# Kernel tuning notes

Hardware: AMD Instinct MI355X
Metric: run time of the kernel (lower is better)

Reference implementation:

```python
import jax, jax.numpy as jnp
import numpy as np

E = 768
H = 12
D = E // H  # head_dim = 64
EPS = 1e-6
SCALE = D ** -0.5


def _l2norm(x, eps=EPS):
    # torch F.normalize: x / clamp_min(||x||_2, eps)
    n = jnp.sqrt(jnp.sum(x * x, axis=-1, keepdims=True))
    return x / jnp.maximum(n, eps)


def setup_inputs() -> dict:
    key = jax.random.key(0)
    ks = jax.random.split(key, 12)
    B, S = 2, 2048
    w = lambda k: jax.random.normal(k, (E, E), dtype=jnp.float32) * 0.02
    b = lambda k: jax.random.normal(k, (E,), dtype=jnp.float32) * 0.02
    return {
        "query": jax.random.normal(ks[0], (B, S, E), dtype=jnp.float32),
        "key": jax.random.normal(ks[1], (B, S, E), dtype=jnp.float32),
        "value": jax.random.normal(ks[2], (B, S, E), dtype=jnp.float32),
        "Wq": w(ks[3]), "bq": b(ks[4]),
        "Wk": w(ks[5]), "bk": b(ks[6]),
        "Wv": w(ks[7]), "bv": b(ks[8]),
        "Wo": w(ks[9]), "bo": b(ks[10]),
    }


def reference(query, key, value, Wq, bq, Wk, bk, Wv, bv, Wo, bo):
    B, T, _ = query.shape
    S = key.shape[1]
    # nn.Linear: x @ W.T + b; then split heads -> [B, H, S, D]
    split = lambda x, L: x.reshape(B, L, H, D).transpose(0, 2, 1, 3)
    q = split(query @ Wq.T + bq, T)
    k = split(key @ Wk.T + bk, S)
    v = split(value @ Wv.T + bv, S)
    q = _l2norm(q)
    k = _l2norm(k)
    scores = jnp.einsum("bhtd,bhsd->bhts", q, k) * SCALE
    attn = jax.nn.softmax(scores, axis=-1)
    ctx = jnp.einsum("bhts,bhsd->bhtd", attn, v)
    ctx = ctx.transpose(0, 2, 1, 3).reshape(B, T, E)
    return ctx @ Wo.T + bo
```

## Files before the change

kernel.cpp:

```cpp
#include <hip/hip_runtime.h>
#include <hip/hip_bf16.h>

#define EE 768
#define HH 12
#define DD 64
#define BB 2
#define SS 2048
#define MM (BB*SS)
#define NT (MM*EE)
#define NW (EE*EE)

typedef short short8 __attribute__((ext_vector_type(8)));
typedef float f32x4 __attribute__((ext_vector_type(4)));

static __device__ __forceinline__ unsigned short f2bf(float f) {
    unsigned int u = __float_as_uint(f);
    u += 0x7fffu + ((u >> 16) & 1u);
    return (unsigned short)(u >> 16);
}

static __device__ __forceinline__ void gl16(const void* g, void* l) {
    __builtin_amdgcn_global_load_lds(
        (const __attribute__((address_space(1))) unsigned int*)g,
        (__attribute__((address_space(3))) unsigned int*)l, 16, 0, 0);
}

static __device__ __forceinline__ int swz(int row, int chunk) {
    return row * 128 + ((chunk ^ (row & 7)) << 4);
}

__global__ __launch_bounds__(256) void cvt_all_kernel(
    const float* __restrict__ xq, const float* __restrict__ xk, const float* __restrict__ xv,
    const float* __restrict__ wq, const float* __restrict__ wk,
    const float* __restrict__ wv, const float* __restrict__ wo,
    unsigned short* __restrict__ oq, unsigned short* __restrict__ ok, unsigned short* __restrict__ ov,
    unsigned short* __restrict__ owq, unsigned short* __restrict__ owk,
    unsigned short* __restrict__ owv, unsigned short* __restrict__ owo)
{
    const int XQ = NT / 4;
    const int WQ = NW / 4;
    const int idx = blockIdx.x * 256 + threadIdx.x;
    const float* s;
    unsigned short* d;
    int off;
    if (idx < 3 * XQ) {
        const int r = idx / XQ;
        off = idx - r * XQ;
        s = (r == 0) ? xq : (r == 1) ? xk : xv;
        d = (r == 0) ? oq : (r == 1) ? ok : ov;
    } else {
        const int j = idx - 3 * XQ;
        const int r = j / WQ;
        off = j - r * WQ;
        s = (r == 0) ? wq : (r == 1) ? wk : (r == 2) ? wv : wo;
        d = (r == 0) ? owq : (r == 1) ? owk : (r == 2) ? owv : owo;
    }
    float4 f = ((const float4*)s)[off];
    ushort4 u;
    u.x = f2bf(f.x); u.y = f2bf(f.y); u.z = f2bf(f.z); u.w = f2bf(f.w);
    ((ushort4*)d)[off] = u;
}

static __device__ __forceinline__ void stage_ab(
    const unsigned short* __restrict__ x, const unsigned short* __restrict__ W,
    int bm, int n0, int kt, short* Abuf, short* Bbuf, int w, int lr8, int lc8)
{
    #pragma unroll
    for (int i = 0; i < 4; ++i) {
        const int t = w * 4 + i;
        gl16(x + (size_t)(bm + t * 8 + lr8) * EE + kt + lc8 * 8,
             (unsigned short*)Abuf + t * 512);
    }
    #pragma unroll
    for (int i = 0; i < 2; ++i) {
        const int t = w * 2 + i;
        gl16(W + (size_t)(n0 + t * 8 + lr8) * EE + kt + lc8 * 8,
             (unsigned short*)Bbuf + t * 512);
    }
}

__global__ __launch_bounds__(256) void qkv_mfma_kernel(
    const unsigned short* __restrict__ xq, const unsigned short* __restrict__ xk,
    const unsigned short* __restrict__ xv,
    const unsigned short* __restrict__ Wq, const float* __restrict__ bq,
    const unsigned short* __restrict__ Wk, const float* __restrict__ bk,
    const unsigned short* __restrict__ Wv, const float* __restrict__ bv,
    unsigned short* __restrict__ qo, unsigned short* __restrict__ ko,
    unsigned short* __restrict__ vo)
{
    __shared__ short As[2][128 * 64];
    __shared__ short Bs[2][64 * 64];
    __shared__ float ssq[2][128];

    const int tid = threadIdx.x;
    const int bm  = blockIdx.x * 128;
    const int by  = blockIdx.y;
    const int proj = by / 12;
    const int h    = by % 12;
    const int n0r  = h * 64;

    const unsigned short* x = (proj == 0) ? xq : (proj == 1) ? xk : xv;
    const unsigned short* W = (proj == 0) ? Wq : (proj == 1) ? Wk : Wv;
    const float* bias       = (proj == 0) ? bq : (proj == 1) ? bk : bv;

    const int w  = tid >> 6;
    const int l  = tid & 63;
    const int c  = l & 15;
    const int g  = l >> 4;
    const int wm = w >> 1;
    const int wn = w & 1;
    const int lr8 = l >> 3;
    const int lc8 = (l & 7) ^ lr8;

    f32x4 acc[4][2] = {};

    stage_ab(x, W, bm, n0r, 0, As[0], Bs[0], w, lr8, lc8);
    __syncthreads();

    for (int it = 0; it < EE / 64; ++it) {
        const int cur = it & 1;
        if (it + 1 < EE / 64)
            stage_ab(x, W, bm, n0r, (it + 1) * 64, As[cur ^ 1], Bs[cur ^ 1], w, lr8, lc8);

        #pragma unroll
        for (int ks = 0; ks < 2; ++ks) {
            short8 bfr[2], afr[4];
            #pragma unroll
            for (int nt = 0; nt < 2; ++nt)
                bfr[nt] = *(const short8*)((const char*)Bs[cur] + swz(wn * 32 + nt * 16 + c, ks * 4 + g));
            #pragma unroll
            for (int mt = 0; mt < 4; ++mt)
                afr[mt] = *(const short8*)((const char*)As[cur] + swz(wm * 64 + mt * 16 + c, ks * 4 + g));
            #pragma unroll
            for (int mt = 0; mt < 4; ++mt)
                #pragma unroll
                for (int nt = 0; nt < 2; ++nt)
                    acc[mt][nt] = __builtin_amdgcn_mfma_f32_16x16x32_bf16(
                        afr[mt], bfr[nt], acc[mt][nt], 0, 0, 0);
        }
        __syncthreads();
    }

    float bb[2];
    #pragma unroll
    for (int nt = 0; nt < 2; ++nt) bb[nt] = bias[n0r + wn * 32 + nt * 16 + c];

    const int bidx  = bm >> 11;
    const int sbase = bm & (SS - 1);

    if (proj < 2) {
        f32x4 vr[4][2];
        f32x4 ssp[4];
        #pragma unroll
        for (int mt = 0; mt < 4; ++mt) {
            #pragma unroll
            for (int nt = 0; nt < 2; ++nt)
                #pragma unroll
                for (int j = 0; j < 4; ++j)
                    vr[mt][nt][j] = acc[mt][nt][j] + bb[nt];
            #pragma unroll
            for (int j = 0; j < 4; ++j)
                ssp[mt][j] = vr[mt][0][j]*vr[mt][0][j] + vr[mt][1][j]*vr[mt][1][j];
            #pragma unroll
            for (int j = 0; j < 4; ++j) {
                float s = ssp[mt][j];
                #pragma unroll
                for (int msk = 1; msk < 16; msk <<= 1) s += __shfl_xor(s, msk);
                ssp[mt][j] = s;
            }
        }
        if (c == 0) {
            #pragma unroll
            for (int mt = 0; mt < 4; ++mt)
                #pragma unroll
                for (int j = 0; j < 4; ++j)
                    ssq[wn][wm * 64 + mt * 16 + g * 4 + j] = ssp[mt][j];
        }
        __syncthreads();
        unsigned short* dst = (proj == 0) ? qo : ko;
        const float fold = (proj == 0) ? 0.125f : 1.0f;
        #pragma unroll
        for (int mt = 0; mt < 4; ++mt) {
            #pragma unroll
            for (int j = 0; j < 4; ++j) {
                const int rloc = wm * 64 + mt * 16 + g * 4 + j;
                const float ss = ssq[0][rloc] + ssq[1][rloc];
                const float inv = fold / fmaxf(sqrtf(ss), 1e-6f);
                const size_t base =
                    ((size_t)(bidx * HH + h) * SS + sbase + rloc) * DD;
                #pragma unroll
                for (int nt = 0; nt < 2; ++nt)
                    dst[base + wn * 32 + nt * 16 + c] = f2bf(vr[mt][nt][j] * inv);
            }
        }
    } else {
        short* T = As[0];
        #pragma unroll
        for (int mt = 0; mt < 4; ++mt)
            #pragma unroll
            for (int nt = 0; nt < 2; ++nt)
                #pragma unroll
                for (int j = 0; j < 4; ++j) {
                    const int row = wm * 64 + mt * 16 + g * 4 + j;
                    const int col = wn * 32 + nt * 16 + c;
                    T[row * 64 + col] = (short)f2bf(acc[mt][nt][j] + bb[nt]);
                }
        __syncthreads();
        const int d  = tid & 63;
        const int sb = (tid >> 6) * 32;
        unsigned short* dstp = vo + ((size_t)(bidx * HH + h) * DD + d) * SS + sbase + sb;
        #pragma unroll
        for (int grp = 0; grp < 4; ++grp) {
            unsigned int wds[4];
            #pragma unroll
            for (int e = 0; e < 4; ++e) {
                unsigned short u0 = (unsigned short)T[(sb + grp * 8 + 2 * e)     * 64 + d];
                unsigned short u1 = (unsigned short)T[(sb + grp * 8 + 2 * e + 1) * 64 + d];
                wds[e] = (unsigned int)u0 | ((unsigned int)u1 << 16);
            }
            int4 pk = make_int4((int)wds[0], (int)wds[1], (int)wds[2], (int)wds[3]);
            *(int4*)(dstp + grp * 8) = pk;
        }
    }
}

static __device__ __forceinline__ void stage_kv(
    const unsigned short* __restrict__ kbase, const unsigned short* __restrict__ vbase,
    int s0, short* Kbuf, short* Vbuf, int w, int lr8, int lc8)
{
    #pragma unroll
    for (int i = 0; i < 4; ++i) {
        const int t = w * 4 + i;
        gl16(kbase + (size_t)(s0 + t * 8 + lr8) * DD + lc8 * 8,
             (unsigned short*)Kbuf + t * 512);
    }
    #pragma unroll
    for (int i = 0; i < 4; ++i) {
        const int t = w * 4 + i;
        gl16(vbase + (size_t)(t * 8 + lr8) * SS + s0 + lc8 * 8,
             (unsigned short*)Vbuf + t * 512);
    }
}

__global__ __launch_bounds__(128) void attn_mfma_kernel(
    const unsigned short* __restrict__ q, const unsigned short* __restrict__ k,
    const unsigned short* __restrict__ vT, unsigned short* __restrict__ ctx)
{
    __shared__ short Ks[2][64 * 64];
    __shared__ short Vs[2][64 * 64];
    __shared__ short Ps[2 * 32 * 64];

    const int tid = threadIdx.x;
    const int bh  = blockIdx.y;
    const int w   = tid >> 6;
    const int l   = tid & 63;
    const int c   = l & 15;
    const int g   = l >> 4;
    const int lr8 = l >> 3;
    const int lc8 = (l & 7) ^ lr8;
    const int qr0 = blockIdx.x * 64 + w * 32;

    const unsigned short* kbase = k  + (size_t)bh * SS * DD;
    const unsigned short* vbase = vT + (size_t)bh * DD * SS;

    short8 aq[2][2];
    #pragma unroll
    for (int m = 0; m < 2; ++m) {
        const unsigned short* qg = q + ((size_t)bh * SS + qr0 + m * 16 + c) * DD;
        aq[m][0] = *(const short8*)(qg + g * 8);
        aq[m][1] = *(const short8*)(qg + 32 + g * 8);
    }

    short* Psw = Ps + w * (32 * 64);
    f32x4 o[2][4] = {};
    f32x4 lsum[2] = {};

    stage_kv(kbase, vbase, 0, Ks[0], Vs[0], w, lr8, lc8);
    __syncthreads();

    for (int t = 0; t < SS / 64; ++t) {
        const int cur = t & 1;
        if (t + 1 < SS / 64)
            stage_kv(kbase, vbase, (t + 1) * 64, Ks[cur ^ 1], Vs[cur ^ 1], w, lr8, lc8);

        f32x4 sc[2][4] = {};
        #pragma unroll
        for (int ks = 0; ks < 2; ++ks)
            #pragma unroll
            for (int nt = 0; nt < 4; ++nt) {
                short8 kf = *(const short8*)((const char*)Ks[cur] + swz(nt * 16 + c, ks * 4 + g));
                #pragma unroll
                for (int m = 0; m < 2; ++m)
                    sc[m][nt] = __builtin_amdgcn_mfma_f32_16x16x32_bf16(
                        aq[m][ks], kf, sc[m][nt], 0, 0, 0);
            }

        #pragma unroll
        for (int m = 0; m < 2; ++m) {
            f32x4 p[4];
            #pragma unroll
            for (int nt = 0; nt < 4; ++nt)
                #pragma unroll
                for (int j = 0; j < 4; ++j)
                    p[nt][j] = __expf(sc[m][nt][j]);
            #pragma unroll
            for (int j = 0; j < 4; ++j) {
                float r = p[0][j] + p[1][j] + p[2][j] + p[3][j];
                #pragma unroll
                for (int msk = 1; msk < 16; msk <<= 1) r += __shfl_xor(r, msk);
                lsum[m][j] += r;
            }
            #pragma unroll
            for (int nt = 0; nt < 4; ++nt)
                #pragma unroll
                for (int j = 0; j < 4; ++j) {
                    const int row = m * 16 + g * 4 + j;
                    const int ch  = (nt * 2 + (c >> 3)) ^ (row & 7);
                    Psw[row * 64 + (ch << 3) + (c & 7)] = (short)f2bf(p[nt][j]);
                }
        }

        #pragma unroll
        for (int ks = 0; ks < 2; ++ks) {
            short8 pa[2];
            #pragma unroll
            for (int m = 0; m < 2; ++m)
                pa[m] = *(const short8*)((const char*)Psw + swz(m * 16 + c, ks * 4 + g));
            #pragma unroll
            for (int dt = 0; dt < 4; ++dt) {
                short8 vf = *(const short8*)((const char*)Vs[cur] + swz(dt * 16 + c, ks * 4 + g));
                #pragma unroll
                for (int m = 0; m < 2; ++m)
                    o[m][dt] = __builtin_amdgcn_mfma_f32_16x16x32_bf16(
                        pa[m], vf, o[m][dt], 0, 0, 0);
            }
        }
        __syncthreads();
    }

    const int bidx = bh / HH, h = bh % HH;
    #pragma unroll
    for (int m = 0; m < 2; ++m)
        #pragma unroll
        for (int j = 0; j < 4; ++j) {
            const float inv = 1.0f / lsum[m][j];
            const int sg = qr0 + m * 16 + g * 4 + j;
            unsigned short* op = ctx + ((size_t)bidx * SS + sg) * EE + h * DD + c;
            #pragma unroll
            for (int dt = 0; dt < 4; ++dt)
                op[dt * 16] = f2bf(o[m][dt][j] * inv);
        }
}

__global__ __launch_bounds__(256) void out_mfma_kernel(
    const unsigned short* __restrict__ A, const unsigned short* __restrict__ W,
    const float* __restrict__ bias, float* __restrict__ out)
{
    __shared__ short As[2][128 * 64];
    __shared__ short Bs[2][64 * 64];

    const int tid = threadIdx.x;
    const int bm  = blockIdx.x * 128;
    const int n0  = blockIdx.y * 64;

    const int w  = tid >> 6;
    const int l  = tid & 63;
    const int c  = l & 15;
    const int g  = l >> 4;
    const int wm = w >> 1;
    const int wn = w & 1;
    const int lr8 = l >> 3;
    const int lc8 = (l & 7) ^ lr8;

    f32x4 acc[4][2] = {};

    stage_ab(A, W, bm, n0, 0, As[0], Bs[0], w, lr8, lc8);
    __syncthreads();

    for (int it = 0; it < EE / 64; ++it) {
        const int cur = it & 1;
        if (it + 1 < EE / 64)
            stage_ab(A, W, bm, n0, (it + 1) * 64, As[cur ^ 1], Bs[cur ^ 1], w, lr8, lc8);

        #pragma unroll
        for (int ks = 0; ks < 2; ++ks) {
            short8 bfr[2], afr[4];
            #pragma unroll
            for (int nt = 0; nt < 2; ++nt)
                bfr[nt] = *(const short8*)((const char*)Bs[cur] + swz(wn * 32 + nt * 16 + c, ks * 4 + g));
            #pragma unroll
            for (int mt = 0; mt < 4; ++mt)
                afr[mt] = *(const short8*)((const char*)As[cur] + swz(wm * 64 + mt * 16 + c, ks * 4 + g));
            #pragma unroll
            for (int mt = 0; mt < 4; ++mt)
                #pragma unroll
                for (int nt = 0; nt < 2; ++nt)
                    acc[mt][nt] = __builtin_amdgcn_mfma_f32_16x16x32_bf16(
                        afr[mt], bfr[nt], acc[mt][nt], 0, 0, 0);
        }
        __syncthreads();
    }

    float bb[2];
    #pragma unroll
    for (int nt = 0; nt < 2; ++nt) bb[nt] = bias[n0 + wn * 32 + nt * 16 + c];

    #pragma unroll
    for (int mt = 0; mt < 4; ++mt)
        #pragma unroll
        for (int j = 0; j < 4; ++j) {
            const int row = bm + wm * 64 + mt * 16 + g * 4 + j;
            float* op = out + (size_t)row * EE + n0 + wn * 32 + c;
            #pragma unroll
            for (int nt = 0; nt < 2; ++nt)
                op[nt * 16] = acc[mt][nt][j] + bb[nt];
        }
}

extern "C" void kernel_launch(void* const* d_in, const int* in_sizes, int n_in,
                              void* d_out, int out_size, void* d_ws, size_t ws_size,
                              hipStream_t stream)
{
    const float* query = (const float*)d_in[0];
    const float* key   = (const float*)d_in[1];
    const float* value = (const float*)d_in[2];
    const float* Wq = (const float*)d_in[3];
    const float* bq = (const float*)d_in[4];
    const float* Wk = (const float*)d_in[5];
    const float* bk = (const float*)d_in[6];
    const float* Wv = (const float*)d_in[7];
    const float* bv = (const float*)d_in[8];
    const float* Wo = (const float*)d_in[9];
    const float* bo = (const float*)d_in[10];
    float* out = (float*)d_out;

    unsigned short* xqc  = (unsigned short*)d_ws;
    unsigned short* xkc  = xqc  + NT;
    unsigned short* xvc  = xkc  + NT;
    unsigned short* qws  = xvc  + NT;
    unsigned short* kws  = qws  + NT;
    unsigned short* vtws = kws  + NT;
    unsigned short* wqc  = vtws + NT;
    unsigned short* wkc  = wqc  + NW;
    unsigned short* wvc  = wkc  + NW;
    unsigned short* woc  = wvc  + NW;
    unsigned short* ctx  = xqc;

    const int cvt_blocks = (3 * (NT / 4) + 4 * (NW / 4)) / 256;
    cvt_all_kernel<<<dim3(cvt_blocks), 256, 0, stream>>>(
        query, key, value, Wq, Wk, Wv, Wo,
        xqc, xkc, xvc, wqc, wkc, wvc, woc);
    qkv_mfma_kernel<<<dim3(MM / 128, 36), 256, 0, stream>>>(
        xqc, xkc, xvc, wqc, bq, wkc, bk, wvc, bv, qws, kws, vtws);
    attn_mfma_kernel<<<dim3(SS / 64, BB * HH), 128, 0, stream>>>(
        qws, kws, vtws, ctx);
    out_mfma_kernel<<<dim3(MM / 128, EE / 64), 256, 0, stream>>>(
        ctx, woc, bo, out);
}
```

Before: 234.6 us.

## Single-buffer GEMM tiles, widen attention to 4 waves, use exp2 and MFMA row sums

The QKV and output GEMMs drop LDS double-buffering in favour of a single buffer with sync-load-sync per K step. This halves shared memory so more blocks can reside on a CU, at the cost of no longer overlapping loads with compute. The attention kernel moves to 256 threads, each wave owning 16 query rows, and folds log2(e) into the Q scale so it can call exp2. Row sums are now taken with an MFMA against a ones vector instead of shuffle reductions, which rounds P to bf16 before summing.

```diff
diff --git a/kernel.cpp b/kernel.cpp
--- a/kernel.cpp
+++ b/kernel.cpp
@@ -61,24 +61,6 @@
     ((ushort4*)d)[off] = u;
 }
 
-static __device__ __forceinline__ void stage_ab(
-    const unsigned short* __restrict__ x, const unsigned short* __restrict__ W,
-    int bm, int n0, int kt, short* Abuf, short* Bbuf, int w, int lr8, int lc8)
-{
-    #pragma unroll
-    for (int i = 0; i < 4; ++i) {
-        const int t = w * 4 + i;
-        gl16(x + (size_t)(bm + t * 8 + lr8) * EE + kt + lc8 * 8,
-             (unsigned short*)Abuf + t * 512);
-    }
-    #pragma unroll
-    for (int i = 0; i < 2; ++i) {
-        const int t = w * 2 + i;
-        gl16(W + (size_t)(n0 + t * 8 + lr8) * EE + kt + lc8 * 8,
-             (unsigned short*)Bbuf + t * 512);
-    }
-}
-
 __global__ __launch_bounds__(256) void qkv_mfma_kernel(
     const unsigned short* __restrict__ xq, const unsigned short* __restrict__ xk,
     const unsigned short* __restrict__ xv,
@@ -88,8 +70,8 @@
     unsigned short* __restrict__ qo, unsigned short* __restrict__ ko,
     unsigned short* __restrict__ vo)
 {
-    __shared__ short As[2][128 * 64];
-    __shared__ short Bs[2][64 * 64];
+    __shared__ short As[128 * 64];
+    __shared__ short Bs[64 * 64];
     __shared__ float ssq[2][128];
 
     const int tid = threadIdx.x;
@@ -114,23 +96,31 @@
 
     f32x4 acc[4][2] = {};
 
-    stage_ab(x, W, bm, n0r, 0, As[0], Bs[0], w, lr8, lc8);
-    __syncthreads();
-
-    for (int it = 0; it < EE / 64; ++it) {
-        const int cur = it & 1;
-        if (it + 1 < EE / 64)
-            stage_ab(x, W, bm, n0r, (it + 1) * 64, As[cur ^ 1], Bs[cur ^ 1], w, lr8, lc8);
+    for (int kt = 0; kt < EE; kt += 64) {
+        __syncthreads();
+        #pragma unroll
+        for (int i = 0; i < 4; ++i) {
+            const int t = w * 4 + i;
+            gl16(x + (size_t)(bm + t * 8 + lr8) * EE + kt + lc8 * 8,
+                 (unsigned short*)As + t * 512);
+        }
+        #pragma unroll
+        for (int i = 0; i < 2; ++i) {
+            const int t = w * 2 + i;
+            gl16(W + (size_t)(n0r + t * 8 + lr8) * EE + kt + lc8 * 8,
+                 (unsigned short*)Bs + t * 512);
+        }
+        __syncthreads();
 
         #pragma unroll
         for (int ks = 0; ks < 2; ++ks) {
             short8 bfr[2], afr[4];
             #pragma unroll
             for (int nt = 0; nt < 2; ++nt)
-                bfr[nt] = *(const short8*)((const char*)Bs[cur] + swz(wn * 32 + nt * 16 + c, ks * 4 + g));
+                bfr[nt] = *(const short8*)((const char*)Bs + swz(wn * 32 + nt * 16 + c, ks * 4 + g));
             #pragma unroll
             for (int mt = 0; mt < 4; ++mt)
-                afr[mt] = *(const short8*)((const char*)As[cur] + swz(wm * 64 + mt * 16 + c, ks * 4 + g));
+                afr[mt] = *(const short8*)((const char*)As + swz(wm * 64 + mt * 16 + c, ks * 4 + g));
             #pragma unroll
             for (int mt = 0; mt < 4; ++mt)
                 #pragma unroll
@@ -138,8 +128,8 @@
                     acc[mt][nt] = __builtin_amdgcn_mfma_f32_16x16x32_bf16(
                         afr[mt], bfr[nt], acc[mt][nt], 0, 0, 0);
         }
-        __syncthreads();
-    }
+    }
+    __syncthreads();
 
     float bb[2];
     #pragma unroll
@@ -178,7 +168,7 @@
         }
         __syncthreads();
         unsigned short* dst = (proj == 0) ? qo : ko;
-        const float fold = (proj == 0) ? 0.125f : 1.0f;
+        const float fold = (proj == 0) ? 0.18033688f : 1.0f;
         #pragma unroll
         for (int mt = 0; mt < 4; ++mt) {
             #pragma unroll
@@ -194,7 +184,6 @@
             }
         }
     } else {
-        short* T = As[0];
         #pragma unroll
         for (int mt = 0; mt < 4; ++mt)
             #pragma unroll
@@ -203,7 +192,7 @@
                 for (int j = 0; j < 4; ++j) {
                     const int row = wm * 64 + mt * 16 + g * 4 + j;
                     const int col = wn * 32 + nt * 16 + c;
-                    T[row * 64 + col] = (short)f2bf(acc[mt][nt][j] + bb[nt]);
+                    As[row * 64 + col] = (short)f2bf(acc[mt][nt][j] + bb[nt]);
                 }
         __syncthreads();
         const int d  = tid & 63;
@@ -214,8 +203,8 @@
             unsigned int wds[4];
             #pragma unroll
             for (int e = 0; e < 4; ++e) {
-                unsigned short u0 = (unsigned short)T[(sb + grp * 8 + 2 * e)     * 64 + d];
-                unsigned short u1 = (unsigned short)T[(sb + grp * 8 + 2 * e + 1) * 64 + d];
+                unsigned short u0 = (unsigned short)As[(sb + grp * 8 + 2 * e)     * 64 + d];
+                unsigned short u1 = (unsigned short)As[(sb + grp * 8 + 2 * e + 1) * 64 + d];
                 wds[e] = (unsigned int)u0 | ((unsigned int)u1 << 16);
             }
             int4 pk = make_int4((int)wds[0], (int)wds[1], (int)wds[2], (int)wds[3]);
@@ -224,31 +213,31 @@
     }
 }
 
-static __device__ __forceinline__ void stage_kv(
+static __device__ __forceinline__ void stage_kv4(
     const unsigned short* __restrict__ kbase, const unsigned short* __restrict__ vbase,
     int s0, short* Kbuf, short* Vbuf, int w, int lr8, int lc8)
 {
     #pragma unroll
-    for (int i = 0; i < 4; ++i) {
-        const int t = w * 4 + i;
+    for (int i = 0; i < 2; ++i) {
+        const int t = w * 2 + i;
         gl16(kbase + (size_t)(s0 + t * 8 + lr8) * DD + lc8 * 8,
              (unsigned short*)Kbuf + t * 512);
     }
     #pragma unroll
-    for (int i = 0; i < 4; ++i) {
-        const int t = w * 4 + i;
+    for (int i = 0; i < 2; ++i) {
+        const int t = w * 2 + i;
         gl16(vbase + (size_t)(t * 8 + lr8) * SS + s0 + lc8 * 8,
              (unsigned short*)Vbuf + t * 512);
     }
 }
 
-__global__ __launch_bounds__(128) void attn_mfma_kernel(
+__global__ __launch_bounds__(256) void attn_mfma_kernel(
     const unsigned short* __restrict__ q, const unsigned short* __restrict__ k,
     const unsigned short* __restrict__ vT, unsigned short* __restrict__ ctx)
 {
     __shared__ short Ks[2][64 * 64];
     __shared__ short Vs[2][64 * 64];
-    __shared__ short Ps[2 * 32 * 64];
+    __shared__ short Ps[4][16 * 64];
 
     const int tid = threadIdx.x;
     const int bh  = blockIdx.y;
@@ -258,81 +247,59 @@
     const int g   = l >> 4;
     const int lr8 = l >> 3;
     const int lc8 = (l & 7) ^ lr8;
-    const int qr0 = blockIdx.x * 64 + w * 32;
+    const int qr0 = blockIdx.x * 64 + w * 16;
 
     const unsigned short* kbase = k  + (size_t)bh * SS * DD;
     const unsigned short* vbase = vT + (size_t)bh * DD * SS;
 
-    short8 aq[2][2];
-    #pragma unroll
-    for (int m = 0; m < 2; ++m) {
-        const unsigned short* qg = q + ((size_t)bh * SS + qr0 + m * 16 + c) * DD;
-        aq[m][0] = *(const short8*)(qg + g * 8);
-        aq[m][1] = *(const short8*)(qg + 32 + g * 8);
-    }
-
-    short* Psw = Ps + w * (32 * 64);
-    f32x4 o[2][4] = {};
-    f32x4 lsum[2] = {};
-
-    stage_kv(kbase, vbase, 0, Ks[0], Vs[0], w, lr8, lc8);
+    short8 aq[2];
+    {
+        const unsigned short* qg = q + ((size_t)bh * SS + qr0 + c) * DD;
+        aq[0] = *(const short8*)(qg + g * 8);
+        aq[1] = *(const short8*)(qg + 32 + g * 8);
+    }
+    const short one_bf = (short)0x3F80;
+    short8 ones = {one_bf, one_bf, one_bf, one_bf, one_bf, one_bf, one_bf, one_bf};
+
+    short* Psw = Ps[w];
+    f32x4 o[4] = {};
+    f32x4 lacc = {0.f, 0.f, 0.f, 0.f};
+
+    stage_kv4(kbase, vbase, 0, Ks[0], Vs[0], w, lr8, lc8);
     __syncthreads();
 
     for (int t = 0; t < SS / 64; ++t) {
         const int cur = t & 1;
         if (t + 1 < SS / 64)
-            stage_kv(kbase, vbase, (t + 1) * 64, Ks[cur ^ 1], Vs[cur ^ 1], w, lr8, lc8);
-
-        f32x4 sc[2][4] = {};
+            stage_kv4(kbase, vbase, (t + 1) * 64, Ks[cur ^ 1], Vs[cur ^ 1], w, lr8, lc8);
+
+        f32x4 sc[4] = {};
         #pragma unroll
         for (int ks = 0; ks < 2; ++ks)
             #pragma unroll
             for (int nt = 0; nt < 4; ++nt) {
                 short8 kf = *(const short8*)((const char*)Ks[cur] + swz(nt * 16 + c, ks * 4 + g));
-                #pragma unroll
-                for (int m = 0; m < 2; ++m)
-                    sc[m][nt] = __builtin_amdgcn_mfma_f32_16x16x32_bf16(
-                        aq[m][ks], kf, sc[m][nt], 0, 0, 0);
-            }
-
-        #pragma unroll
-        for (int m = 0; m < 2; ++m) {
-            f32x4 p[4];
-            #pragma unroll
-            for (int nt = 0; nt < 4; ++nt)
-                #pragma unroll
-                for (int j = 0; j < 4; ++j)
-                    p[nt][j] = __expf(sc[m][nt][j]);
+                sc[nt] = __builtin_amdgcn_mfma_f32_16x16x32_bf16(aq[ks], kf, sc[nt], 0, 0, 0);
+            }
+
+        #pragma unroll
+        for (int nt = 0; nt < 4; ++nt)
             #pragma unroll
             for (int j = 0; j < 4; ++j) {
-                float r = p[0][j] + p[1][j] + p[2][j] + p[3][j];
-                #pragma unroll
-                for (int msk = 1; msk < 16; msk <<= 1) r += __shfl_xor(r, msk);
-                lsum[m][j] += r;
-            }
-            #pragma unroll
-            for (int nt = 0; nt < 4; ++nt)
-                #pragma unroll
-                for (int j = 0; j < 4; ++j) {
-                    const int row = m * 16 + g * 4 + j;
-                    const int ch  = (nt * 2 + (c >> 3)) ^ (row & 7);
-                    Psw[row * 64 + (ch << 3) + (c & 7)] = (short)f2bf(p[nt][j]);
-                }
-        }
+                const float p = __builtin_exp2f(sc[nt][j]);
+                const int row = g * 4 + j;
+                const int ch  = (nt * 2 + (c >> 3)) ^ (row & 7);
+                Psw[row * 64 + (ch << 3) + (c & 7)] = (short)f2bf(p);
+            }
 
         #pragma unroll
         for (int ks = 0; ks < 2; ++ks) {
-            short8 pa[2];
-            #pragma unroll
-            for (int m = 0; m < 2; ++m)
-                pa[m] = *(const short8*)((const char*)Psw + swz(m * 16 + c, ks * 4 + g));
+            short8 pa = *(const short8*)((const char*)Psw + swz(c, ks * 4 + g));
+            lacc = __builtin_amdgcn_mfma_f32_16x16x32_bf16(pa, ones, lacc, 0, 0, 0);
             #pragma unroll
             for (int dt = 0; dt < 4; ++dt) {
                 short8 vf = *(const short8*)((const char*)Vs[cur] + swz(dt * 16 + c, ks * 4 + g));
-                #pragma unroll
-                for (int m = 0; m < 2; ++m)
-                    o[m][dt] = __builtin_amdgcn_mfma_f32_16x16x32_bf16(
-                        pa[m], vf, o[m][dt], 0, 0, 0);
+                o[dt] = __builtin_amdgcn_mfma_f32_16x16x32_bf16(pa, vf, o[dt], 0, 0, 0);
             }
         }
         __syncthreads();
@@ -340,24 +307,22 @@
 
     const int bidx = bh / HH, h = bh % HH;
     #pragma unroll
-    for (int m = 0; m < 2; ++m)
-        #pragma unroll
-        for (int j = 0; j < 4; ++j) {
-            const float inv = 1.0f / lsum[m][j];
-            const int sg = qr0 + m * 16 + g * 4 + j;
-            unsigned short* op = ctx + ((size_t)bidx * SS + sg) * EE + h * DD + c;
-            #pragma unroll
-            for (int dt = 0; dt < 4; ++dt)
-                op[dt * 16] = f2bf(o[m][dt][j] * inv);
-        }
+    for (int j = 0; j < 4; ++j) {
+        const float inv = 1.0f / lacc[j];
+        const int sg = qr0 + g * 4 + j;
+        unsigned short* op = ctx + ((size_t)bidx * SS + sg) * EE + h * DD + c;
+        #pragma unroll
+        for (int dt = 0; dt < 4; ++dt)
+            op[dt * 16] = f2bf(o[dt][j] * inv);
+    }
 }
 
 __global__ __launch_bounds__(256) void out_mfma_kernel(
     const unsigned short* __restrict__ A, const unsigned short* __restrict__ W,
     const float* __restrict__ bias, float* __restrict__ out)
 {
-    __shared__ short As[2][128 * 64];
-    __shared__ short Bs[2][64 * 64];
+    __shared__ short As[128 * 64];
+    __shared__ short Bs[64 * 64];
 
     const int tid = threadIdx.x;
     const int bm  = blockIdx.x * 128;
@@ -374,23 +339,31 @@
 
     f32x4 acc[4][2] = {};
 
-    stage_ab(A, W, bm, n0, 0, As[0], Bs[0], w, lr8, lc8);
-    __syncthreads();
-
-    for (int it = 0; it < EE / 64; ++it) {
-        const int cur = it & 1;
-        if (it + 1 < EE / 64)
-            stage_ab(A, W, bm, n0, (it + 1) * 64, As[cur ^ 1], Bs[cur ^ 1], w, lr8, lc8);
+    for (int kt = 0; kt < EE; kt += 64) {
+        __syncthreads();
+        #pragma unroll
+        for (int i = 0; i < 4; ++i) {
+            const int t = w * 4 + i;
+            gl16(A + (size_t)(bm + t * 8 + lr8) * EE + kt + lc8 * 8,
+                 (unsigned short*)As + t * 512);
+        }
+        #pragma unroll
+        for (int i = 0; i < 2; ++i) {
+            const int t = w * 2 + i;
+            gl16(W + (size_t)(n0 + t * 8 + lr8) * EE + kt + lc8 * 8,
+                 (unsigned short*)Bs + t * 512);
+        }
+        __syncthreads();
 
         #pragma unroll
         for (int ks = 0; ks < 2; ++ks) {
             short8 bfr[2], afr[4];
             #pragma unroll
             for (int nt = 0; nt < 2; ++nt)
-                bfr[nt] = *(const short8*)((const char*)Bs[cur] + swz(wn * 32 + nt * 16 + c, ks * 4 + g));
+                bfr[nt] = *(const short8*)((const char*)Bs + swz(wn * 32 + nt * 16 + c, ks * 4 + g));
             #pragma unroll
             for (int mt = 0; mt < 4; ++mt)
-                afr[mt] = *(const short8*)((const char*)As[cur] + swz(wm * 64 + mt * 16 + c, ks * 4 + g));
+                afr[mt] = *(const short8*)((const char*)As + swz(wm * 64 + mt * 16 + c, ks * 4 + g));
             #pragma unroll
             for (int mt = 0; mt < 4; ++mt)
                 #pragma unroll
@@ -398,7 +371,6 @@
                     acc[mt][nt] = __builtin_amdgcn_mfma_f32_16x16x32_bf16(
                         afr[mt], bfr[nt], acc[mt][nt], 0, 0, 0);
         }
-        __syncthreads();
     }
 
     float bb[2];
@@ -452,7 +424,7 @@
         xqc, xkc, xvc, wqc, wkc, wvc, woc);
     qkv_mfma_kernel<<<dim3(MM / 128, 36), 256, 0, stream>>>(
         xqc, xkc, xvc, wqc, bq, wkc, bk, wvc, bv, qws, kws, vtws);
-    attn_mfma_kernel<<<dim3(SS / 64, BB * HH), 128, 0, stream>>>(
+    attn_mfma_kernel<<<dim3(SS / 64, BB * HH), 256, 0, stream>>>(
         qws, kws, vtws, ctx);
     out_mfma_kernel<<<dim3(MM / 128, EE / 64), 256, 0, stream>>>(
         ctx, woc, bo, out);
```

Result: faster. 202.5 us (-13.7%).
